# Performance work log

Hardware: AMD Instinct MI355X
Metric: run time of the kernel (lower is better)

Reference implementation:

```python
import jax, jax.numpy as jnp
import numpy as np

B, E, CIN, C, H, W = 8, 16, 64, 64, 64, 64


def setup_inputs() -> dict:
    key = jax.random.key(0)
    ks = jax.random.split(key, 7)
    in_tensor = jax.random.normal(ks[0], (B, E, CIN, H, W), dtype=jnp.float32)
    # 1x1 conv weights are [out_channels, in_channels]; biases [out_channels]
    s = 1.0 / np.sqrt(CIN)
    Wv = jax.random.normal(ks[1], (C, CIN), dtype=jnp.float32) * s
    bv = jax.random.normal(ks[2], (C,), dtype=jnp.float32) * 0.01
    Wk = jax.random.normal(ks[3], (C, CIN), dtype=jnp.float32) * s
    bk = jax.random.normal(ks[4], (C,), dtype=jnp.float32) * 0.01
    Wq = jax.random.normal(ks[5], (C, CIN), dtype=jnp.float32) * s
    bq = jax.random.normal(ks[6], (C,), dtype=jnp.float32) * 0.01
    return {"in_tensor": in_tensor, "Wv": Wv, "bv": bv, "Wk": Wk, "bk": bk, "Wq": Wq, "bq": bq}


def _ens_conv1x1(x, Wt, b):
    # EnsConv2d: 1x1 conv applied to every ensemble member independently
    # x: [b, i(ens), a(in_ch), h, w] -> [b, i, c(out_ch), h, w]
    return jnp.einsum('biahw,ca->bichw', x, Wt) + b[None, None, :, None, None]


def reference(in_tensor, Wv, bv, Wk, bk, Wq, bq):
    value = _ens_conv1x1(in_tensor, Wv, bv)
    key_t = jax.nn.selu(_ens_conv1x1(in_tensor, Wk, bk))
    query = jax.nn.selu(_ens_conv1x1(in_tensor, Wq, bq))
    # gram matrix over ensemble members, per (batch, channel)
    dots = jnp.einsum('bichw,bjchw->bcij', key_t, query)  # [b,c,i,j]
    # softmax over key axis i (summed-out axis in _apply_weights)
    weights = jax.nn.softmax(dots, axis=-2)
    # mean-centered weighted combine of ensemble perturbations
    value_mean = jnp.mean(value, axis=1, keepdims=True)  # [b,1,c,h,w]
    value_perts = value - value_mean
    transformed_perts = jnp.einsum('bcij,bichw->bjchw', weights, value_perts)
    out = jax.nn.selu(value_mean + transformed_perts)
    return out
```

## Files before the change

kernel.cpp:

```cpp
#include <hip/hip_runtime.h>
#include <cstdint>
#include <cstddef>

#define B_   8
#define E_   16
#define CIN_ 64
#define C_   64
#define HW_  4096

typedef __attribute__((ext_vector_type(8))) short short8;
typedef __attribute__((ext_vector_type(4))) float floatx4;

__device__ __forceinline__ float selu_f(float v) {
    const float kAlphaScale = 1.7580993408473766f;
    const float kScale      = 1.0507009873554805f;
    return v > 0.0f ? kScale * v : kAlphaScale * (__expf(v) - 1.0f);
}

__device__ __forceinline__ unsigned short f2bf(float f) {
    unsigned int u = __float_as_uint(f);
    u += 0x7fffu + ((u >> 16) & 1u);
    return (unsigned short)(u >> 16);
}
__device__ __forceinline__ float bf2f(unsigned short h) {
    return __uint_as_float(((unsigned int)h) << 16);
}

__device__ __forceinline__ void stage_w_sw(const float* __restrict__ W,
                                           unsigned short* Wh, unsigned short* Wl, int t) {
    for (int idx = t; idx < 4096; idx += 256) {
        const int c = idx >> 6, k = idx & 63;
        const int o = c * 64 + (k ^ ((c & 7) << 3));
        const float f = W[idx];
        const unsigned short h = f2bf(f);
        Wh[o] = h;
        Wl[o] = f2bf(f - bf2f(h));
    }
}
__device__ __forceinline__ void stage_w_hi(const float* __restrict__ W,
                                           unsigned short* Wh, int t) {
    for (int idx = t; idx < 4096; idx += 256) {
        const int c = idx >> 6, k = idx & 63;
        Wh[c * 64 + (k ^ ((c & 7) << 3))] = f2bf(W[idx]);
    }
}

#define WPAD 72
__device__ __forceinline__ void stage_w(const float* __restrict__ W,
                                        unsigned short* Wh, unsigned short* Wl, int t) {
    for (int idx = t; idx < 4096; idx += 256) {
        const int c = idx >> 6, k = idx & 63;
        const float f = W[idx];
        const unsigned short h = f2bf(f);
        Wh[c * WPAD + k] = h;
        Wl[c * WPAD + k] = f2bf(f - bf2f(h));
    }
}

#define K1_CH 4
#define KCS 18
#define KIS 292

__global__ __launch_bounds__(256, 2)
void dots_kernel(const float* __restrict__ x,
                 const float* __restrict__ Wk, const float* __restrict__ bk,
                 const float* __restrict__ Wq, const float* __restrict__ bq,
                 const float* __restrict__ Wv, const float* __restrict__ bv,
                 unsigned short* __restrict__ vbuf,
                 float* __restrict__ wts, float* __restrict__ part,
                 int use_atomic)
{
    __shared__ float sK[E_ * KIS];
    __shared__ float sQ[E_ * KIS];
    __shared__ __align__(16) unsigned short Wkh[4096], Wkl[4096];
    __shared__ __align__(16) unsigned short Wqh[4096], Wql[4096];
    __shared__ __align__(16) unsigned short Wvh[4096];

    const int t    = threadIdx.x;
    const int b    = blockIdx.x >> 6;
    const int blk  = blockIdx.x & 63;
    const int wv   = t >> 6;
    const int lane = t & 63;
    const int quad = lane >> 4;
    const int pxl  = lane & 15;
    const int m16  = lane & 15;
    const int gc = t >> 4;
    const int s  = t & 15;
    const int ib = (s >> 2) << 2;
    const int jb = (s & 3) << 2;

    stage_w_sw(Wk, Wkh, Wkl, t);
    stage_w_sw(Wq, Wqh, Wql, t);
    if (vbuf) stage_w_hi(Wv, Wvh, t);

    float acc[4][4][4];
    #pragma unroll
    for (int a0 = 0; a0 < 4; ++a0)
      #pragma unroll
      for (int a1 = 0; a1 < 4; ++a1)
        #pragma unroll
        for (int a2 = 0; a2 < 4; ++a2) acc[a0][a1][a2] = 0.0f;

    __syncthreads();

    for (int chunk = 0; chunk < K1_CH; ++chunk) {
        const int p0 = blk * (16 * K1_CH) + chunk * 16;

        short8 xh[4][2], xl[4][2];
        #pragma unroll
        for (int mi = 0; mi < 4; ++mi) {
            const int im = 4 * wv + mi;
            const float* xg = x + ((size_t)(b * E_ + im) * CIN_) * HW_ + p0 + pxl;
            #pragma unroll
            for (int kk = 0; kk < 2; ++kk) {
                float xv[8];
                #pragma unroll
                for (int j = 0; j < 8; ++j)
                    xv[j] = xg[(size_t)(kk * 32 + quad * 8 + j) * HW_];
                #pragma unroll
                for (int j = 0; j < 8; ++j) {
                    const unsigned short h = f2bf(xv[j]);
                    xh[mi][kk][j] = (short)h;
                    xl[mi][kk][j] = (short)f2bf(xv[j] - bf2f(h));
                }
            }
        }

        for (int q4 = 0; q4 < 4; ++q4) {
            const int row = q4 * 16 + m16;
            const int ksw = (row & 7) << 3;

            if (vbuf) {
                short8 vh[2];
                #pragma unroll
                for (int kk = 0; kk < 2; ++kk) {
                    const int k0 = kk * 32 + quad * 8;
                    vh[kk] = *(const short8*)&Wvh[row * 64 + (k0 ^ ksw)];
                }
                float bvv[4];
                #pragma unroll
                for (int r = 0; r < 4; ++r) bvv[r] = bv[q4 * 16 + quad * 4 + r];
                #pragma unroll
                for (int mi = 0; mi < 4; ++mi) {
                    floatx4 d = {0.f, 0.f, 0.f, 0.f};
                    d = __builtin_amdgcn_mfma_f32_16x16x32_bf16(vh[0], xh[mi][0], d, 0, 0, 0);
                    d = __builtin_amdgcn_mfma_f32_16x16x32_bf16(vh[0], xl[mi][0], d, 0, 0, 0);
                    d = __builtin_amdgcn_mfma_f32_16x16x32_bf16(vh[1], xh[mi][1], d, 0, 0, 0);
                    d = __builtin_amdgcn_mfma_f32_16x16x32_bf16(vh[1], xl[mi][1], d, 0, 0, 0);
                    const int im = 4 * wv + mi;
                    #pragma unroll
                    for (int r = 0; r < 4; ++r)
                        vbuf[((size_t)(b * E_ + im) * C_ + (q4 * 16 + quad * 4 + r)) * HW_ + p0 + pxl]
                            = f2bf(d[r] + bvv[r]);
                }
            }

            {
                short8 ah[2], al[2];
                #pragma unroll
                for (int kk = 0; kk < 2; ++kk) {
                    const int k0 = kk * 32 + quad * 8;
                    const int off = row * 64 + (k0 ^ ksw);
                    ah[kk] = *(const short8*)&Wkh[off];
                    al[kk] = *(const short8*)&Wkl[off];
                }
                float bkv[4];
                #pragma unroll
                for (int r = 0; r < 4; ++r) bkv[r] = bk[q4 * 16 + quad * 4 + r];
                #pragma unroll
                for (int mi = 0; mi < 4; ++mi) {
                    floatx4 d = {0.f, 0.f, 0.f, 0.f};
                    #pragma unroll
                    for (int kk = 0; kk < 2; ++kk) {
                        d = __builtin_amdgcn_mfma_f32_16x16x32_bf16(ah[kk], xh[mi][kk], d, 0, 0, 0);
                        d = __builtin_amdgcn_mfma_f32_16x16x32_bf16(ah[kk], xl[mi][kk], d, 0, 0, 0);
                        d = __builtin_amdgcn_mfma_f32_16x16x32_bf16(al[kk], xh[mi][kk], d, 0, 0, 0);
                    }
                    const int im = 4 * wv + mi;
                    #pragma unroll
                    for (int r = 0; r < 4; ++r)
                        sK[im * KIS + (quad * 4 + r) * KCS + pxl] = selu_f(d[r] + bkv[r]);
                }
            }
            {
                short8 ah[2], al[2];
                #pragma unroll
                for (int kk = 0; kk < 2; ++kk) {
                    const int k0 = kk * 32 + quad * 8;
                    const int off = row * 64 + (k0 ^ ksw);
                    ah[kk] = *(const short8*)&Wqh[off];
                    al[kk] = *(const short8*)&Wql[off];
                }
                float bqv[4];
                #pragma unroll
                for (int r = 0; r < 4; ++r) bqv[r] = bq[q4 * 16 + quad * 4 + r];
                #pragma unroll
                for (int mi = 0; mi < 4; ++mi) {
                    floatx4 d = {0.f, 0.f, 0.f, 0.f};
                    #pragma unroll
                    for (int kk = 0; kk < 2; ++kk) {
                        d = __builtin_amdgcn_mfma_f32_16x16x32_bf16(ah[kk], xh[mi][kk], d, 0, 0, 0);
                        d = __builtin_amdgcn_mfma_f32_16x16x32_bf16(ah[kk], xl[mi][kk], d, 0, 0, 0);
                        d = __builtin_amdgcn_mfma_f32_16x16x32_bf16(al[kk], xh[mi][kk], d, 0, 0, 0);
                    }
                    const int im = 4 * wv + mi;
                    #pragma unroll
                    for (int r = 0; r < 4; ++r)
                        sQ[im * KIS + (quad * 4 + r) * KCS + pxl] = selu_f(d[r] + bqv[r]);
                }
            }
            __syncthreads();
            #pragma unroll
            for (int p2 = 0; p2 < 8; ++p2) {
                float2 kv[4], qv[4];
                #pragma unroll
                for (int u = 0; u < 4; ++u)
                    kv[u] = *(const float2*)&sK[(ib + u) * KIS + gc * KCS + 2 * p2];
                #pragma unroll
                for (int v = 0; v < 4; ++v)
                    qv[v] = *(const float2*)&sQ[(jb + v) * KIS + gc * KCS + 2 * p2];
                #pragma unroll
                for (int u = 0; u < 4; ++u)
                    #pragma unroll
                    for (int v = 0; v < 4; ++v)
                        acc[q4][u][v] = __fmaf_rn(kv[u].y, qv[v].y,
                                         __fmaf_rn(kv[u].x, qv[v].x, acc[q4][u][v]));
            }
            __syncthreads();
        }
    }

    if (use_atomic) {
        #pragma unroll
        for (int q4 = 0; q4 < 4; ++q4)
          #pragma unroll
          for (int u = 0; u < 4; ++u)
            #pragma unroll
            for (int v = 0; v < 4; ++v)
              atomicAdd(&wts[(((size_t)b * C_ + (q4 * 16 + gc)) * E_ + (ib + u)) * E_ + (jb + v)],
                        acc[q4][u][v]);
    } else {
        float* pb = part + (size_t)blockIdx.x * (C_ * E_ * E_);
        #pragma unroll
        for (int q4 = 0; q4 < 4; ++q4) {
            __syncthreads();
            #pragma unroll
            for (int u = 0; u < 4; ++u)
              #pragma unroll
              for (int v = 0; v < 4; ++v)
                sK[gc * 256 + (ib + u) * 16 + (jb + v)] = acc[q4][u][v];
            __syncthreads();
            for (int e = t; e < 4096; e += 256)
                pb[q4 * 4096 + e] = sK[e];
        }
    }
}

__global__ __launch_bounds__(256)
void reduce_kernel(const float* __restrict__ part, float* __restrict__ wts)
{
    const int tid = blockIdx.x * 256 + threadIdx.x;
    const int b   = tid >> 12;
    const int off = tid & 4095;
    float4 sum = make_float4(0.f, 0.f, 0.f, 0.f);
    const float* base = part + (size_t)b * 64 * 16384;
    #pragma unroll 8
    for (int blk = 0; blk < 64; ++blk) {
        float4 v = *(const float4*)(base + (size_t)blk * 16384 + off * 4);
        sum.x += v.x; sum.y += v.y; sum.z += v.z; sum.w += v.w;
    }
    *(float4*)(wts + (size_t)b * 16384 + off * 4) = sum;
}

__global__ __launch_bounds__(256)
void softmax_kernel(float* __restrict__ wts)
{
    const int tid = blockIdx.x * 256 + threadIdx.x;
    const int j   = tid & 15;
    const int bc  = tid >> 4;
    float* base = wts + (size_t)bc * 256 + j;
    float v[16];
    #pragma unroll
    for (int i = 0; i < 16; ++i) v[i] = base[i * 16];
    float m = v[0];
    #pragma unroll
    for (int i = 1; i < 16; ++i) m = fmaxf(m, v[i]);
    float sum = 0.f;
    #pragma unroll
    for (int i = 0; i < 16; ++i) { v[i] = __expf(v[i] - m); sum += v[i]; }
    const float r = 1.0f / sum;
    #pragma unroll
    for (int i = 0; i < 16; ++i) base[i * 16] = v[i] * r;
}

#define VCS 20
#define VIS 1284

__global__ __launch_bounds__(256, 2)
void combine_kernel(const unsigned short* __restrict__ vbuf,
                    const float* __restrict__ wts, float* __restrict__ out)
{
    __shared__ __align__(16) unsigned short sV[E_ * VIS];

    const int t   = threadIdx.x;
    const int b   = blockIdx.x >> 6;
    const int blk = blockIdx.x & 63;
    const int c   = t >> 2;
    const int q   = t & 3;

    for (int chunk = 0; chunk < 4; ++chunk) {
        const int p0 = blk * 64 + chunk * 16;

        if (chunk) __syncthreads();
        for (int idx = t; idx < 2048; idx += 256) {
            const int i    = idx >> 7;
            const int rest = idx & 127;
            const int cc   = rest >> 1;
            const int h    = rest & 1;
            const uint4 u = *(const uint4*)(vbuf +
                (((size_t)(b * E_ + i) * C_ + cc) * HW_ + p0 + h * 8));
            unsigned short* dst = &sV[i * VIS + cc * VCS + h * 8];
            *(uint2*)dst       = make_uint2(u.x, u.y);
            *(uint2*)(dst + 4) = make_uint2(u.z, u.w);
        }
        __syncthreads();

        float acc2[4][16];
        #pragma unroll
        for (int jj = 0; jj < 4; ++jj)
            #pragma unroll
            for (int pp = 0; pp < 16; ++pp) acc2[jj][pp] = 0.f;

        #pragma unroll 4
        for (int i2 = 0; i2 < 16; ++i2) {
            const float4 w4 = *(const float4*)&wts[(((size_t)b * C_ + c) * E_ + i2) * E_ + 4 * q];
            const unsigned short* vp = &sV[i2 * VIS + c * VCS];
            float vvv[16];
            #pragma unroll
            for (int pq = 0; pq < 4; ++pq) {
                const uint2 u = *(const uint2*)(vp + 4 * pq);
                vvv[4 * pq + 0] = __uint_as_float(u.x << 16);
                vvv[4 * pq + 1] = __uint_as_float(u.x & 0xffff0000u);
                vvv[4 * pq + 2] = __uint_as_float(u.y << 16);
                vvv[4 * pq + 3] = __uint_as_float(u.y & 0xffff0000u);
            }
            const float wj0 = w4.x, wj1 = w4.y, wj2 = w4.z, wj3 = w4.w;
            #pragma unroll
            for (int pp = 0; pp < 16; ++pp) {
                acc2[0][pp] = __fmaf_rn(wj0, vvv[pp], acc2[0][pp]);
                acc2[1][pp] = __fmaf_rn(wj1, vvv[pp], acc2[1][pp]);
                acc2[2][pp] = __fmaf_rn(wj2, vvv[pp], acc2[2][pp]);
                acc2[3][pp] = __fmaf_rn(wj3, vvv[pp], acc2[3][pp]);
            }
        }

        #pragma unroll
        for (int jj = 0; jj < 4; ++jj) {
            const int j = 4 * q + jj;
            float* op = out + ((size_t)((b * E_ + j) * C_ + c)) * HW_ + p0;
            #pragma unroll
            for (int pq = 0; pq < 4; ++pq) {
                float4 o;
                o.x = selu_f(acc2[jj][4 * pq + 0]);
                o.y = selu_f(acc2[jj][4 * pq + 1]);
                o.z = selu_f(acc2[jj][4 * pq + 2]);
                o.w = selu_f(acc2[jj][4 * pq + 3]);
                *(float4*)(op + 4 * pq) = o;
            }
        }
    }
}

#define K3_CH 2

__global__ __launch_bounds__(256, 2)
void out_kernel(const float* __restrict__ x,
                const float* __restrict__ Wv, const float* __restrict__ bv,
                const float* __restrict__ wts, float* __restrict__ out)
{
    __shared__ __align__(16) unsigned short sV[E_ * VIS];
    __shared__ __align__(16) unsigned short Wvh[64 * WPAD], Wvl[64 * WPAD];

    const int t    = threadIdx.x;
    const int b    = blockIdx.x >> 7;
    const int blk  = blockIdx.x & 127;
    const int wv   = t >> 6;
    const int lane = t & 63;
    const int quad = lane >> 4;
    const int pxl  = lane & 15;
    const int m16  = lane & 15;
    const int c    = t >> 2;
    const int q    = t & 3;

    stage_w(Wv, Wvh, Wvl, t);
    __syncthreads();

    for (int chunk = 0; chunk < K3_CH; ++chunk) {
        const int p0 = blk * (16 * K3_CH) + chunk * 16;

        short8 xh[4][2], xl[4][2];
        #pragma unroll
        for (int mi = 0; mi < 4; ++mi) {
            const int im = 4 * wv + mi;
            const float* xg = x + ((size_t)(b * E_ + im) * CIN_) * HW_ + p0 + pxl;
            #pragma unroll
            for (int kk = 0; kk < 2; ++kk) {
                float xv[8];
                #pragma unroll
                for (int j = 0; j < 8; ++j)
                    xv[j] = xg[(size_t)(kk * 32 + quad * 8 + j) * HW_];
                #pragma unroll
                for (int j = 0; j < 8; ++j) {
                    const unsigned short h = f2bf(xv[j]);
                    xh[mi][kk][j] = (short)h;
                    xl[mi][kk][j] = (short)f2bf(xv[j] - bf2f(h));
                }
            }
        }

        #pragma unroll
        for (int cb = 0; cb < 4; ++cb) {
            short8 ah[2], al[2];
            #pragma unroll
            for (int kk = 0; kk < 2; ++kk) {
                const int off = (cb * 16 + m16) * WPAD + kk * 32 + quad * 8;
                ah[kk] = *(const short8*)&Wvh[off];
                al[kk] = *(const short8*)&Wvl[off];
            }
            float bvv[4];
            #pragma unroll
            for (int r = 0; r < 4; ++r) bvv[r] = bv[cb * 16 + quad * 4 + r];
            #pragma unroll
            for (int mi = 0; mi < 4; ++mi) {
                floatx4 d = {0.f, 0.f, 0.f, 0.f};
                #pragma unroll
                for (int kk = 0; kk < 2; ++kk) {
                    d = __builtin_amdgcn_mfma_f32_16x16x32_bf16(ah[kk], xh[mi][kk], d, 0, 0, 0);
                    d = __builtin_amdgcn_mfma_f32_16x16x32_bf16(ah[kk], xl[mi][kk], d, 0, 0, 0);
                    d = __builtin_amdgcn_mfma_f32_16x16x32_bf16(al[kk], xh[mi][kk], d, 0, 0, 0);
                }
                const int im = 4 * wv + mi;
                #pragma unroll
                for (int r = 0; r < 4; ++r)
                    sV[im * VIS + (cb * 16 + quad * 4 + r) * VCS + pxl] = f2bf(d[r] + bvv[r]);
            }
        }
        __syncthreads();

        float acc2[4][16];
        #pragma unroll
        for (int jj = 0; jj < 4; ++jj)
            #pragma unroll
            for (int pp = 0; pp < 16; ++pp) acc2[jj][pp] = 0.f;

        #pragma unroll 4
        for (int i2 = 0; i2 < 16; ++i2) {
            const float4 w4 = *(const float4*)&wts[(((size_t)b * C_ + c) * E_ + i2) * E_ + 4 * q];
            const unsigned short* vp = &sV[i2 * VIS + c * VCS];
            float vvv[16];
            #pragma unroll
            for (int pq = 0; pq < 4; ++pq) {
                const uint2 u = *(const uint2*)(vp + 4 * pq);
                vvv[4 * pq + 0] = __uint_as_float(u.x << 16);
                vvv[4 * pq + 1] = __uint_as_float(u.x & 0xffff0000u);
                vvv[4 * pq + 2] = __uint_as_float(u.y << 16);
                vvv[4 * pq + 3] = __uint_as_float(u.y & 0xffff0000u);
            }
            const float wj0 = w4.x, wj1 = w4.y, wj2 = w4.z, wj3 = w4.w;
            #pragma unroll
            for (int pp = 0; pp < 16; ++pp) {
                acc2[0][pp] = __fmaf_rn(wj0, vvv[pp], acc2[0][pp]);
                acc2[1][pp] = __fmaf_rn(wj1, vvv[pp], acc2[1][pp]);
                acc2[2][pp] = __fmaf_rn(wj2, vvv[pp], acc2[2][pp]);
                acc2[3][pp] = __fmaf_rn(wj3, vvv[pp], acc2[3][pp]);
            }
        }

        #pragma unroll
        for (int jj = 0; jj < 4; ++jj) {
            const int j = 4 * q + jj;
            float* op = out + ((size_t)((b * E_ + j) * C_ + c)) * HW_ + p0;
            #pragma unroll
            for (int pq = 0; pq < 4; ++pq) {
                float4 o;
                o.x = selu_f(acc2[jj][4 * pq + 0]);
                o.y = selu_f(acc2[jj][4 * pq + 1]);
                o.z = selu_f(acc2[jj][4 * pq + 2]);
                o.w = selu_f(acc2[jj][4 * pq + 3]);
                *(float4*)(op + 4 * pq) = o;
            }
        }
        __syncthreads();
    }
}

extern "C" void kernel_launch(void* const* d_in, const int* in_sizes, int n_in,
                              void* d_out, int out_size, void* d_ws, size_t ws_size,
                              hipStream_t stream)
{
    (void)in_sizes; (void)n_in; (void)out_size;
    const float* x  = (const float*)d_in[0];
    const float* Wv = (const float*)d_in[1];
    const float* bv = (const float*)d_in[2];
    const float* Wk = (const float*)d_in[3];
    const float* bk = (const float*)d_in[4];
    const float* Wq = (const float*)d_in[5];
    const float* bq = (const float*)d_in[6];
    float* out = (float*)d_out;

    const size_t wts_b  = (size_t)B_ * C_ * E_ * E_ * sizeof(float);
    const size_t part_b = (size_t)512 * C_ * E_ * E_ * sizeof(float);
    const size_t v_b    = (size_t)B_ * E_ * C_ * HW_ * sizeof(unsigned short);

    float* wts = (float*)d_ws;
    float* part = nullptr;
    unsigned short* vbuf = nullptr;
    int use_atomic, have_v;

    if (ws_size >= wts_b + part_b + v_b) {
        use_atomic = 0; have_v = 1;
        part = (float*)((char*)d_ws + wts_b);
        vbuf = (unsigned short*)((char*)d_ws + wts_b + part_b);
    } else if (ws_size >= wts_b + part_b) {
        use_atomic = 0; have_v = 0;
        part = (float*)((char*)d_ws + wts_b);
    } else if (ws_size >= wts_b + v_b) {
        use_atomic = 1; have_v = 1;
        vbuf = (unsigned short*)((char*)d_ws + wts_b);
    } else {
        use_atomic = 1; have_v = 0;
    }

    if (use_atomic)
        hipMemsetAsync(d_ws, 0, wts_b, stream);

    dots_kernel<<<dim3(512), dim3(256), 0, stream>>>(x, Wk, bk, Wq, bq, Wv, bv,
                                                     vbuf, wts, part, use_atomic);
    if (!use_atomic)
        reduce_kernel<<<dim3(128), dim3(256), 0, stream>>>(part, wts);
    softmax_kernel<<<dim3(32), dim3(256), 0, stream>>>(wts);
    if (have_v)
        combine_kernel<<<dim3(512), dim3(256), 0, stream>>>(vbuf, wts, out);
    else
        out_kernel<<<dim3(1024), dim3(256), 0, stream>>>(x, Wv, bv, wts, out);
}
```

Baseline: 521.1 us.

## Store value buffer in pixel-tiled layout and widen combine chunks to 32 pixels

```diff
diff --git a/kernel.cpp b/kernel.cpp
--- a/kernel.cpp
+++ b/kernel.cpp
@@ -105,6 +105,7 @@
 
     for (int chunk = 0; chunk < K1_CH; ++chunk) {
         const int p0 = blk * (16 * K1_CH) + chunk * 16;
+        const size_t tb = ((size_t)((b * 64 + blk) * 4 + chunk)) * 16384;
 
         short8 xh[4][2], xl[4][2];
         #pragma unroll
@@ -150,7 +151,7 @@
                     const int im = 4 * wv + mi;
                     #pragma unroll
                     for (int r = 0; r < 4; ++r)
-                        vbuf[((size_t)(b * E_ + im) * C_ + (q4 * 16 + quad * 4 + r)) * HW_ + p0 + pxl]
+                        vbuf[tb + im * 1024 + (q4 * 16 + quad * 4 + r) * 16 + pxl]
                             = f2bf(d[r] + bvv[r]);
                 }
             }
@@ -293,14 +294,14 @@
     for (int i = 0; i < 16; ++i) base[i * 16] = v[i] * r;
 }
 
-#define VCS 20
-#define VIS 1284
+#define VCS2 36
+#define SVIS (64 * VCS2)
 
 __global__ __launch_bounds__(256, 2)
 void combine_kernel(const unsigned short* __restrict__ vbuf,
                     const float* __restrict__ wts, float* __restrict__ out)
 {
-    __shared__ __align__(16) unsigned short sV[E_ * VIS];
+    __shared__ __align__(16) unsigned short sV[E_ * SVIS];
 
     const int t   = threadIdx.x;
     const int b   = blockIdx.x >> 6;
@@ -308,49 +309,59 @@
     const int c   = t >> 2;
     const int q   = t & 3;
 
-    for (int chunk = 0; chunk < 4; ++chunk) {
-        const int p0 = blk * 64 + chunk * 16;
-
-        if (chunk) __syncthreads();
-        for (int idx = t; idx < 2048; idx += 256) {
-            const int i    = idx >> 7;
-            const int rest = idx & 127;
-            const int cc   = rest >> 1;
-            const int h    = rest & 1;
-            const uint4 u = *(const uint4*)(vbuf +
-                (((size_t)(b * E_ + i) * C_ + cc) * HW_ + p0 + h * 8));
-            unsigned short* dst = &sV[i * VIS + cc * VCS + h * 8];
-            *(uint2*)dst       = make_uint2(u.x, u.y);
-            *(uint2*)(dst + 4) = make_uint2(u.z, u.w);
+    const size_t tbase = ((size_t)(b * 64 + blk)) * 4 * 16384;
+
+    for (int u = 0; u < 2; ++u) {
+        const int p0 = blk * 64 + u * 32;
+
+        if (u) __syncthreads();
+        #pragma unroll 4
+        for (int it = 0; it < 16; ++it) {
+            const int idx = t + 256 * it;
+            const int g   = idx & 3;
+            const int cc  = (idx >> 2) & 63;
+            const int i   = idx >> 8;
+            const unsigned short* src = vbuf + tbase
+                + (size_t)(2 * u + (g >> 1)) * 16384 + i * 1024 + cc * 16 + (g & 1) * 8;
+            const uint4 v = *(const uint4*)src;
+            unsigned short* dst = &sV[i * SVIS + cc * VCS2 + g * 8];
+            *(uint2*)(dst)     = make_uint2(v.x, v.y);
+            *(uint2*)(dst + 4) = make_uint2(v.z, v.w);
         }
         __syncthreads();
 
-        float acc2[4][16];
+        float acc2[4][32];
         #pragma unroll
         for (int jj = 0; jj < 4; ++jj)
             #pragma unroll
-            for (int pp = 0; pp < 16; ++pp) acc2[jj][pp] = 0.f;
+            for (int pp = 0; pp < 32; ++pp) acc2[jj][pp] = 0.f;
 
         #pragma unroll 4
         for (int i2 = 0; i2 < 16; ++i2) {
             const float4 w4 = *(const float4*)&wts[(((size_t)b * C_ + c) * E_ + i2) * E_ + 4 * q];
-            const unsigned short* vp = &sV[i2 * VIS + c * VCS];
-            float vvv[16];
-            #pragma unroll
-            for (int pq = 0; pq < 4; ++pq) {
-                const uint2 u = *(const uint2*)(vp + 4 * pq);
-                vvv[4 * pq + 0] = __uint_as_float(u.x << 16);
-                vvv[4 * pq + 1] = __uint_as_float(u.x & 0xffff0000u);
-                vvv[4 * pq + 2] = __uint_as_float(u.y << 16);
-                vvv[4 * pq + 3] = __uint_as_float(u.y & 0xffff0000u);
-            }
+            const unsigned short* vp = &sV[i2 * SVIS + c * VCS2];
             const float wj0 = w4.x, wj1 = w4.y, wj2 = w4.z, wj3 = w4.w;
             #pragma unroll
-            for (int pp = 0; pp < 16; ++pp) {
-                acc2[0][pp] = __fmaf_rn(wj0, vvv[pp], acc2[0][pp]);
-                acc2[1][pp] = __fmaf_rn(wj1, vvv[pp], acc2[1][pp]);
-                acc2[2][pp] = __fmaf_rn(wj2, vvv[pp], acc2[2][pp]);
-                acc2[3][pp] = __fmaf_rn(wj3, vvv[pp], acc2[3][pp]);
+            for (int pq8 = 0; pq8 < 4; ++pq8) {
+                const uint2 ua = *(const uint2*)(vp + 8 * pq8);
+                const uint2 ub = *(const uint2*)(vp + 8 * pq8 + 4);
+                float vv[8];
+                vv[0] = __uint_as_float(ua.x << 16);
+                vv[1] = __uint_as_float(ua.x & 0xffff0000u);
+                vv[2] = __uint_as_float(ua.y << 16);
+                vv[3] = __uint_as_float(ua.y & 0xffff0000u);
+                vv[4] = __uint_as_float(ub.x << 16);
+                vv[5] = __uint_as_float(ub.x & 0xffff0000u);
+                vv[6] = __uint_as_float(ub.y << 16);
+                vv[7] = __uint_as_float(ub.y & 0xffff0000u);
+                #pragma unroll
+                for (int k = 0; k < 8; ++k) {
+                    const int pp = 8 * pq8 + k;
+                    acc2[0][pp] = __fmaf_rn(wj0, vv[k], acc2[0][pp]);
+                    acc2[1][pp] = __fmaf_rn(wj1, vv[k], acc2[1][pp]);
+                    acc2[2][pp] = __fmaf_rn(wj2, vv[k], acc2[2][pp]);
+                    acc2[3][pp] = __fmaf_rn(wj3, vv[k], acc2[3][pp]);
+                }
             }
         }
 
@@ -359,19 +370,21 @@
             const int j = 4 * q + jj;
             float* op = out + ((size_t)((b * E_ + j) * C_ + c)) * HW_ + p0;
             #pragma unroll
-            for (int pq = 0; pq < 4; ++pq) {
+            for (int s4 = 0; s4 < 8; ++s4) {
                 float4 o;
-                o.x = selu_f(acc2[jj][4 * pq + 0]);
-                o.y = selu_f(acc2[jj][4 * pq + 1]);
-                o.z = selu_f(acc2[jj][4 * pq + 2]);
-                o.w = selu_f(acc2[jj][4 * pq + 3]);
-                *(float4*)(op + 4 * pq) = o;
+                o.x = selu_f(acc2[jj][4 * s4 + 0]);
+                o.y = selu_f(acc2[jj][4 * s4 + 1]);
+                o.z = selu_f(acc2[jj][4 * s4 + 2]);
+                o.w = selu_f(acc2[jj][4 * s4 + 3]);
+                *(float4*)(op + 4 * s4) = o;
             }
         }
     }
 }
 
 #define K3_CH 2
+#define VCS 20
+#define VIS 1284
 
 __global__ __launch_bounds__(256, 2)
 void out_kernel(const float* __restrict__ x,
```

Result: faster. 508.3 us (-2.4%).

## Store value buffer in pixel-tiled layout and rewrite combine kernel without LDS

Applied to the files above, without the earlier changes.

```diff
diff --git a/kernel.cpp b/kernel.cpp
--- a/kernel.cpp
+++ b/kernel.cpp
@@ -105,6 +105,7 @@
 
     for (int chunk = 0; chunk < K1_CH; ++chunk) {
         const int p0 = blk * (16 * K1_CH) + chunk * 16;
+        const size_t tb = ((size_t)((b * 64 + blk) * 4 + chunk)) * 16384;
 
         short8 xh[4][2], xl[4][2];
         #pragma unroll
@@ -150,7 +151,7 @@
                     const int im = 4 * wv + mi;
                     #pragma unroll
                     for (int r = 0; r < 4; ++r)
-                        vbuf[((size_t)(b * E_ + im) * C_ + (q4 * 16 + quad * 4 + r)) * HW_ + p0 + pxl]
+                        vbuf[tb + im * 1024 + (q4 * 16 + quad * 4 + r) * 16 + pxl]
                             = f2bf(d[r] + bvv[r]);
                 }
             }
@@ -293,85 +294,71 @@
     for (int i = 0; i < 16; ++i) base[i * 16] = v[i] * r;
 }
 
-#define VCS 20
-#define VIS 1284
-
-__global__ __launch_bounds__(256, 2)
+__global__ __launch_bounds__(256, 4)
 void combine_kernel(const unsigned short* __restrict__ vbuf,
                     const float* __restrict__ wts, float* __restrict__ out)
 {
-    __shared__ __align__(16) unsigned short sV[E_ * VIS];
-
     const int t   = threadIdx.x;
-    const int b   = blockIdx.x >> 6;
-    const int blk = blockIdx.x & 63;
-    const int c   = t >> 2;
-    const int q   = t & 3;
-
-    for (int chunk = 0; chunk < 4; ++chunk) {
-        const int p0 = blk * 64 + chunk * 16;
-
-        if (chunk) __syncthreads();
-        for (int idx = t; idx < 2048; idx += 256) {
-            const int i    = idx >> 7;
-            const int rest = idx & 127;
-            const int cc   = rest >> 1;
-            const int h    = rest & 1;
-            const uint4 u = *(const uint4*)(vbuf +
-                (((size_t)(b * E_ + i) * C_ + cc) * HW_ + p0 + h * 8));
-            unsigned short* dst = &sV[i * VIS + cc * VCS + h * 8];
-            *(uint2*)dst       = make_uint2(u.x, u.y);
-            *(uint2*)(dst + 4) = make_uint2(u.z, u.w);
-        }
-        __syncthreads();
-
-        float acc2[4][16];
-        #pragma unroll
-        for (int jj = 0; jj < 4; ++jj)
-            #pragma unroll
-            for (int pp = 0; pp < 16; ++pp) acc2[jj][pp] = 0.f;
-
-        #pragma unroll 4
-        for (int i2 = 0; i2 < 16; ++i2) {
-            const float4 w4 = *(const float4*)&wts[(((size_t)b * C_ + c) * E_ + i2) * E_ + 4 * q];
-            const unsigned short* vp = &sV[i2 * VIS + c * VCS];
-            float vvv[16];
-            #pragma unroll
-            for (int pq = 0; pq < 4; ++pq) {
-                const uint2 u = *(const uint2*)(vp + 4 * pq);
-                vvv[4 * pq + 0] = __uint_as_float(u.x << 16);
-                vvv[4 * pq + 1] = __uint_as_float(u.x & 0xffff0000u);
-                vvv[4 * pq + 2] = __uint_as_float(u.y << 16);
-                vvv[4 * pq + 3] = __uint_as_float(u.y & 0xffff0000u);
-            }
-            const float wj0 = w4.x, wj1 = w4.y, wj2 = w4.z, wj3 = w4.w;
-            #pragma unroll
-            for (int pp = 0; pp < 16; ++pp) {
-                acc2[0][pp] = __fmaf_rn(wj0, vvv[pp], acc2[0][pp]);
-                acc2[1][pp] = __fmaf_rn(wj1, vvv[pp], acc2[1][pp]);
-                acc2[2][pp] = __fmaf_rn(wj2, vvv[pp], acc2[2][pp]);
-                acc2[3][pp] = __fmaf_rn(wj3, vvv[pp], acc2[3][pp]);
-            }
-        }
-
-        #pragma unroll
-        for (int jj = 0; jj < 4; ++jj) {
-            const int j = 4 * q + jj;
-            float* op = out + ((size_t)((b * E_ + j) * C_ + c)) * HW_ + p0;
-            #pragma unroll
-            for (int pq = 0; pq < 4; ++pq) {
-                float4 o;
-                o.x = selu_f(acc2[jj][4 * pq + 0]);
-                o.y = selu_f(acc2[jj][4 * pq + 1]);
-                o.z = selu_f(acc2[jj][4 * pq + 2]);
-                o.w = selu_f(acc2[jj][4 * pq + 3]);
-                *(float4*)(op + 4 * pq) = o;
-            }
-        }
+    const int wv  = t >> 6;
+    const int l   = t & 63;
+    const int bid = blockIdx.x;
+    const int b   = bid >> 10;
+    const int blk = (bid >> 4) & 63;
+    const int cg  = bid & 15;
+    const int c   = cg * 4 + wv;
+
+    const int ih    = l >> 5;
+    const int lx    = l & 31;
+    const int px    = 2 * lx;
+    const int chunk = lx >> 3;
+    const int inpx  = px & 15;
+
+    const unsigned short* vb = vbuf + ((size_t)(b * 64 + blk)) * 65536
+                             + chunk * 16384 + c * 16 + inpx;
+    const float* wb = wts + (((size_t)(b * 64 + c)) * 16) * 16;
+
+    float acc[16][2];
+    #pragma unroll
+    for (int j = 0; j < 16; ++j) { acc[j][0] = 0.f; acc[j][1] = 0.f; }
+
+    #pragma unroll
+    for (int ip = 0; ip < 8; ++ip) {
+        const int i = 2 * ip + ih;
+        const unsigned int u = *(const unsigned int*)(vb + i * 1024);
+        const float f0 = __uint_as_float(u << 16);
+        const float f1 = __uint_as_float(u & 0xffff0000u);
+        const float4* wp4 = (const float4*)(wb + i * 16);
+        const float4 w0 = wp4[0], w1 = wp4[1], w2 = wp4[2], w3 = wp4[3];
+        const float wj[16] = { w0.x, w0.y, w0.z, w0.w,  w1.x, w1.y, w1.z, w1.w,
+                               w2.x, w2.y, w2.z, w2.w,  w3.x, w3.y, w3.z, w3.w };
+        #pragma unroll
+        for (int j = 0; j < 16; ++j) {
+            acc[j][0] = __fmaf_rn(wj[j], f0, acc[j][0]);
+            acc[j][1] = __fmaf_rn(wj[j], f1, acc[j][1]);
+        }
+    }
+
+    #pragma unroll
+    for (int j = 0; j < 16; ++j) {
+        acc[j][0] += __shfl_xor(acc[j][0], 32);
+        acc[j][1] += __shfl_xor(acc[j][1], 32);
+    }
+
+    #pragma unroll
+    for (int jj = 0; jj < 8; ++jj) {
+        const float a0 = ih ? acc[jj + 8][0] : acc[jj][0];
+        const float a1 = ih ? acc[jj + 8][1] : acc[jj][1];
+        float2 o;
+        o.x = selu_f(a0);
+        o.y = selu_f(a1);
+        float* op = out + (((size_t)(b * E_ + jj + 8 * ih) * C_ + c) * HW_) + blk * 64 + px;
+        *(float2*)op = o;
     }
 }
 
 #define K3_CH 2
+#define VCS 20
+#define VIS 1284
 
 __global__ __launch_bounds__(256, 2)
 void out_kernel(const float* __restrict__ x,
@@ -540,7 +527,7 @@
         reduce_kernel<<<dim3(128), dim3(256), 0, stream>>>(part, wts);
     softmax_kernel<<<dim3(32), dim3(256), 0, stream>>>(wts);
     if (have_v)
-        combine_kernel<<<dim3(512), dim3(256), 0, stream>>>(vbuf, wts, out);
+        combine_kernel<<<dim3(8192), dim3(256), 0, stream>>>(vbuf, wts, out);
     else
         out_kernel<<<dim3(1024), dim3(256), 0, stream>>>(x, Wv, bv, wts, out);
 }
```

Measured after the change: 593.0 us. 1.14x slower.
